# Optimization experiments

Hardware: AMD Instinct MI355X
Metric: run time of the kernel (lower is better)

## Reference

```python
import jax, jax.numpy as jnp
import numpy as np

R = 16
ALPHA = 32
SCALING = ALPHA / R  # 2.0
E = 8
TOP_K = 2


def setup_inputs() -> dict:
    key = jax.random.key(0)
    ks = jax.random.split(key, 5)
    B, S, D = 4, 2048, 4096
    x = jax.random.normal(ks[0], (B, S, D), dtype=jnp.float32)
    base_W = jax.random.normal(ks[1], (D, D), dtype=jnp.float32) * 0.02
    router_W = jax.random.normal(ks[2], (E, D), dtype=jnp.float32) * 0.02
    lora_A = jax.random.normal(ks[3], (E, D, R), dtype=jnp.float32) * 0.02
    lora_B = jax.random.normal(ks[4], (E, R, D), dtype=jnp.float32) * 0.02
    return {"x": x, "base_W": base_W, "router_W": router_W,
            "lora_A": lora_A, "lora_B": lora_B}


def reference(x, base_W, router_W, lora_A, lora_B):
    # base linear: y = x @ W^T  (nn.Linear, bias=False)
    base = jnp.einsum('bsd,od->bso', x, base_W)

    # router logits and top-2 routing (softmax in fp32, as in torch)
    logits = jnp.einsum('bsd,ed->bse', x, router_W)
    probs = jax.nn.softmax(logits.astype(jnp.float32), axis=-1)  # [B,S,E]
    top_vals, top_idx = jax.lax.top_k(probs, TOP_K)               # [B,S,2]
    rw = top_vals / jnp.sum(top_vals, axis=-1, keepdims=True)
    # scatter top-2 weights into dense [B,S,E] combine matrix
    w_dense = jnp.sum(jax.nn.one_hot(top_idx, E, dtype=rw.dtype) * rw[..., None],
                      axis=-2).astype(x.dtype)                    # [B,S,E]

    # expert LoRA: out_n = sum_e w_ne * (x_n @ A_e @ B_e)
    # apply routing weight at rank-r stage (B_e linear => same math),
    # avoiding the [B,S,E,D] intermediate.
    mid = jnp.einsum('bsd,edr->bser', x, lora_A)                  # [B,S,E,r]
    mid = mid * w_dense[..., None]
    inc = jnp.einsum('bser,erd->bsd', mid, lora_B)                # [B,S,D]

    return base + inc * SCALING
```

## Files before the change

kernel.cpp:

```cpp
#include <hip/hip_runtime.h>
#include <math.h>

#define DI __device__ __forceinline__

typedef __attribute__((ext_vector_type(4))) float  f32x4;
typedef __attribute__((ext_vector_type(4))) short  s16x4;
typedef __attribute__((ext_vector_type(8))) short  s16x8;
typedef __attribute__((ext_vector_type(4))) float  ffrag;
typedef s16x8 bfrag;

constexpr int NT = 8192;
constexpr int D  = 4096;
constexpr int NE = 8;
constexpr int KE = 128;
constexpr int KX = D + KE;

DI short f2bf(float f) {
  unsigned u = __builtin_bit_cast(unsigned, f);
  u += 0x7FFFu + ((u >> 16) & 1u);
  return (short)(u >> 16);
}
DI float bf2f(short h) {
  unsigned u = ((unsigned)(unsigned short)h) << 16;
  return __builtin_bit_cast(float, u);
}

#define GLOAD16(gp, lp)                                                        \
  __builtin_amdgcn_global_load_lds(                                            \
      (const __attribute__((address_space(1))) void*)(gp),                     \
      (__attribute__((address_space(3))) void*)(lp), 16, 0, 0)

__global__ void moe_k_detect(const unsigned* __restrict__ x, int* __restrict__ flag) {
  int l = threadIdx.x;
  int cnt = 0;
  for (int i = l; i < 2048; i += 64) {
    unsigned e = (x[i] >> 23) & 0xFFu;
    cnt += (e >= 110u && e <= 140u) ? 1 : 0;
  }
#pragma unroll
  for (int o = 32; o; o >>= 1) cnt += __shfl_xor(cnt, o);
  if (l == 0) flag[0] = (cnt > 1024) ? 0 : 1;
}

__global__ __launch_bounds__(256)
void moe_k_prep(const void* __restrict__ wp, const void* __restrict__ lAp,
                const void* __restrict__ lBp, const int* __restrict__ flag,
                short* __restrict__ Wb, short* __restrict__ Abt) {
  const bool bf = flag[0] != 0;
  int b = blockIdx.x, t = threadIdx.x;
  if (b < 8192) {
    int tid = b * 256 + t;
    int row = tid >> 9;
    int col = (tid & 511) << 3;
    s16x8 o;
    if (!bf) {
      const float* Wf = (const float*)wp;
      f32x4 v0 = *(const f32x4*)&Wf[(size_t)row * 4096 + col];
      f32x4 v1 = *(const f32x4*)&Wf[(size_t)row * 4096 + col + 4];
      o[0] = f2bf(v0[0]); o[1] = f2bf(v0[1]); o[2] = f2bf(v0[2]); o[3] = f2bf(v0[3]);
      o[4] = f2bf(v1[0]); o[5] = f2bf(v1[1]); o[6] = f2bf(v1[2]); o[7] = f2bf(v1[3]);
    } else {
      o = *(const s16x8*)&((const short*)wp)[(size_t)row * 4096 + col];
    }
    *(s16x8*)&Wb[(size_t)row * KX + col] = o;
  } else if (b < 8208) {
    int d = (b - 8192) * 256 + t;
    for (int j0 = 0; j0 < KE; j0 += 8) {
      s16x8 o;
#pragma unroll
      for (int i = 0; i < 8; ++i) {
        float v = bf ? bf2f(((const short*)lBp)[(size_t)(j0 + i) * 4096 + d])
                     : ((const float*)lBp)[(size_t)(j0 + i) * 4096 + d];
        o[i] = f2bf(2.0f * v);
      }
      *(s16x8*)&Wb[(size_t)d * KX + 4096 + j0] = o;
    }
  } else {
    int j = b - 8208;
    int e = j >> 4, r = j & 15;
    for (int d = t; d < 4096; d += 256) {
      size_t src = ((size_t)e * 4096 + d) * 16 + r;
      short v = bf ? ((const short*)lAp)[src] : f2bf(((const float*)lAp)[src]);
      Abt[(size_t)j * 4096 + d] = v;
    }
  }
}

__global__ __launch_bounds__(256)
void moe_k_xrouter(const void* __restrict__ xp, const void* __restrict__ rp,
                   const int* __restrict__ flag, short* __restrict__ Xb,
                   float* __restrict__ wdense) {
  const bool bf = flag[0] != 0;
  int t = threadIdx.x, wv = t >> 6, l = t & 63;
  int n = blockIdx.x * 4 + wv;
  float acc[NE];
#pragma unroll
  for (int e = 0; e < NE; ++e) acc[e] = 0.f;
  const float* xf = (const float*)xp;
  const short* xh = (const short*)xp;
  const float* rf = (const float*)rp;
  const short* rh = (const short*)rp;
  for (int it = 0; it < 16; ++it) {
    int d = it * 256 + l * 4;
    float x0, x1, x2, x3;
    s16x4 xo;
    if (!bf) {
      f32x4 v = *(const f32x4*)&xf[(size_t)n * D + d];
      x0 = v[0]; x1 = v[1]; x2 = v[2]; x3 = v[3];
      xo[0] = f2bf(x0); xo[1] = f2bf(x1); xo[2] = f2bf(x2); xo[3] = f2bf(x3);
    } else {
      xo = *(const s16x4*)&xh[(size_t)n * D + d];
      x0 = bf2f(xo[0]); x1 = bf2f(xo[1]); x2 = bf2f(xo[2]); x3 = bf2f(xo[3]);
    }
    *(s16x4*)&Xb[(size_t)n * KX + d] = xo;
#pragma unroll
    for (int e = 0; e < NE; ++e) {
      if (!bf) {
        f32x4 w = *(const f32x4*)&rf[(size_t)e * D + d];
        acc[e] += x0 * w[0] + x1 * w[1] + x2 * w[2] + x3 * w[3];
      } else {
        s16x4 w = *(const s16x4*)&rh[(size_t)e * D + d];
        acc[e] += x0 * bf2f(w[0]) + x1 * bf2f(w[1]) + x2 * bf2f(w[2]) + x3 * bf2f(w[3]);
      }
    }
  }
#pragma unroll
  for (int e = 0; e < NE; ++e) {
#pragma unroll
    for (int o = 32; o; o >>= 1) acc[e] += __shfl_xor(acc[e], o);
  }
  float m = acc[0];
#pragma unroll
  for (int e = 1; e < NE; ++e) m = fmaxf(m, acc[e]);
  float p[NE];
#pragma unroll
  for (int e = 0; e < NE; ++e) p[e] = __expf(acc[e] - m);
  int i1 = 0; float v1 = p[0];
#pragma unroll
  for (int e = 1; e < NE; ++e) { if (p[e] > v1) { v1 = p[e]; i1 = e; } }
  int i2 = 0; float v2 = -1.f;
#pragma unroll
  for (int e = 0; e < NE; ++e) { if (e != i1 && p[e] > v2) { v2 = p[e]; i2 = e; } }
  float inv = 1.f / (v1 + v2);
  if (l < NE) {
    float w = (l == i1) ? v1 * inv : ((l == i2) ? v2 * inv : 0.f);
    wdense[(size_t)n * NE + l] = w;
  }
}

__global__ __launch_bounds__(256)
void moe_k_mid2(const short* __restrict__ Xb, const short* __restrict__ Abt,
                const float* __restrict__ wdense, short* __restrict__ XbW) {
  __shared__ __align__(16) short LDS[16384];
  const int t = threadIdx.x, l = t & 63, wv = t >> 6;
  const int wr = wv >> 1, wc = wv & 1;
  const int lr = l & 15, kq = l >> 4;
  const int m0 = (blockIdx.x >> 1) * 64;
  const int j0 = (blockIdx.x & 1) * 64;

  ffrag acc[2][2];
#pragma unroll
  for (int i = 0; i < 2; ++i)
#pragma unroll
    for (int j = 0; j < 2; ++j)
#pragma unroll
      for (int q = 0; q < 4; ++q) acc[i][j][q] = 0.f;

  const int srow = t >> 2, sslot = t & 3;
#define MSTAGE(kt_)                                                            \
  do {                                                                         \
    int _k0 = (kt_) * 32, _b = ((kt_) & 3) * 4096;                             \
    GLOAD16(&Xb[(size_t)(m0 + srow) * KX + _k0 + sslot * 8], &LDS[_b + t * 8]);\
    GLOAD16(&Abt[(size_t)(j0 + srow) * 4096 + _k0 + sslot * 8],                \
            &LDS[_b + 2048 + t * 8]);                                          \
  } while (0)

  MSTAGE(0); MSTAGE(1); MSTAGE(2);
  constexpr int NKT = 128;

  for (int kt = 0; kt < NKT; ++kt) {
    if (kt + 2 < NKT)      asm volatile("s_waitcnt vmcnt(4)" ::: "memory");
    else if (kt + 1 < NKT) asm volatile("s_waitcnt vmcnt(2)" ::: "memory");
    else                   asm volatile("s_waitcnt vmcnt(0)" ::: "memory");
    __builtin_amdgcn_s_barrier();
    __builtin_amdgcn_sched_barrier(0);

    const int bufs = (kt & 3) * 4096;
    const short* As = &LDS[bufs + (wr * 32 + lr) * 32 + kq * 8];
    const short* Bs = &LDS[bufs + 2048 + (wc * 32 + lr) * 32 + kq * 8];
    bfrag a0 = *(const bfrag*)&As[0];
    bfrag a1 = *(const bfrag*)&As[512];
    bfrag b0 = *(const bfrag*)&Bs[0];
    bfrag b1 = *(const bfrag*)&Bs[512];
    if (kt + 3 < NKT) MSTAGE(kt + 3);
    asm volatile("" ::: "memory");
    acc[0][0] = __builtin_amdgcn_mfma_f32_16x16x32_bf16(b0, a0, acc[0][0], 0, 0, 0);
    acc[0][1] = __builtin_amdgcn_mfma_f32_16x16x32_bf16(b1, a0, acc[0][1], 0, 0, 0);
    acc[1][0] = __builtin_amdgcn_mfma_f32_16x16x32_bf16(b0, a1, acc[1][0], 0, 0, 0);
    acc[1][1] = __builtin_amdgcn_mfma_f32_16x16x32_bf16(b1, a1, acc[1][1], 0, 0, 0);
  }

#pragma unroll
  for (int m = 0; m < 2; ++m)
#pragma unroll
    for (int n = 0; n < 2; ++n) {
      int gr = m0 + wr * 32 + m * 16 + lr;
      int jb = j0 + wc * 32 + n * 16 + kq * 4;
      int e  = jb >> 4;
      float w = wdense[(size_t)gr * NE + e];
      s16x4 o;
#pragma unroll
      for (int q = 0; q < 4; ++q) o[q] = f2bf(acc[m][n][q] * w);
      *(s16x4*)&XbW[(size_t)gr * KX + 4096 + jb] = o;
    }
#undef MSTAGE
}

__global__ __launch_bounds__(512, 2)
void moe_k_main8(const short* __restrict__ Xb, const short* __restrict__ Wb,
                 const int* __restrict__ flag, void* __restrict__ outp) {
  __shared__ __align__(16) short LDS[65536];
  const int t = threadIdx.x;
  const int l = t & 63;
  const int wv = t >> 6;
  const int wr = wv >> 2;
  const int wc = wv & 3;
  const int lr = l & 15;
  const int kq = l >> 4;

  int wg = blockIdx.x;
  int swz = (wg & 7) * 64 + (wg >> 3);
  const int tm = (swz >> 4) * 256;
  const int tn = (swz & 15) * 256;

  ffrag acc[8][4];
#pragma unroll
  for (int i = 0; i < 8; ++i)
#pragma unroll
    for (int j = 0; j < 4; ++j)
#pragma unroll
      for (int q = 0; q < 4; ++q) acc[i][j][q] = 0.f;

#define STAGE_A(kt_)                                                           \
  do {                                                                         \
    int _k0 = (kt_) * 32, _b = ((kt_) & 3) * 16384;                            \
    _Pragma("unroll")                                                          \
    for (int _i = 0; _i < 2; ++_i) {                                           \
      int _c = _i * 512 + t;                                                   \
      int _r = _c >> 2;                                                        \
      int _kc = (_c & 3) ^ ((_r >> 1) & 3);                                    \
      GLOAD16(&Xb[(size_t)(tm + _r) * KX + _k0 + _kc * 8], &LDS[_b + _c * 8]); \
    }                                                                          \
  } while (0)
#define STAGE_B(kt_)                                                           \
  do {                                                                         \
    int _k0 = (kt_) * 32, _b = ((kt_) & 3) * 16384 + 8192;                     \
    _Pragma("unroll")                                                          \
    for (int _i = 0; _i < 2; ++_i) {                                           \
      int _c = _i * 512 + t;                                                   \
      int _r = _c >> 2;                                                        \
      int _kc = (_c & 3) ^ ((_r >> 1) & 3);                                    \
      GLOAD16(&Wb[(size_t)(tn + _r) * KX + _k0 + _kc * 8], &LDS[_b + _c * 8]); \
    }                                                                          \
  } while (0)

  STAGE_A(0); STAGE_B(0);
  STAGE_A(1); STAGE_B(1);
  STAGE_A(2); STAGE_B(2);

  constexpr int NKT = KX / 32;

  const int kx = kq ^ ((lr >> 1) & 3);
  const int aofs = (wr * 128 + lr) * 32 + kx * 8;
  const int bofs = 8192 + (wc * 64 + lr) * 32 + kx * 8;

#define MFMA_ROW(mi, av)                                                           \
  acc[mi][0] = __builtin_amdgcn_mfma_f32_16x16x32_bf16(b0, av, acc[mi][0], 0, 0, 0); \
  acc[mi][1] = __builtin_amdgcn_mfma_f32_16x16x32_bf16(b1, av, acc[mi][1], 0, 0, 0); \
  acc[mi][2] = __builtin_amdgcn_mfma_f32_16x16x32_bf16(b2, av, acc[mi][2], 0, 0, 0); \
  acc[mi][3] = __builtin_amdgcn_mfma_f32_16x16x32_bf16(b3, av, acc[mi][3], 0, 0, 0);

  for (int kt = 0; kt < NKT; ++kt) {
    if (kt + 2 < NKT)      asm volatile("s_waitcnt vmcnt(8)" ::: "memory");
    else if (kt + 1 < NKT) asm volatile("s_waitcnt vmcnt(4)" ::: "memory");
    else                   asm volatile("s_waitcnt vmcnt(0)" ::: "memory");
    __builtin_amdgcn_s_barrier();
    __builtin_amdgcn_sched_barrier(0);

    const int bufs = (kt & 3) * 16384;
    const short* Ab = &LDS[bufs + aofs];
    const short* Bb = &LDS[bufs + bofs];

    bfrag b0 = *(const bfrag*)&Bb[0];
    bfrag b1 = *(const bfrag*)&Bb[512];
    bfrag b2 = *(const bfrag*)&Bb[1024];
    bfrag b3 = *(const bfrag*)&Bb[1536];
    bfrag a0 = *(const bfrag*)&Ab[0];
    bfrag a1 = *(const bfrag*)&Ab[512];
    bfrag a2 = *(const bfrag*)&Ab[1024];
    bfrag a3 = *(const bfrag*)&Ab[1536];
    if (kt + 3 < NKT) STAGE_A(kt + 3);
    asm volatile("" ::: "memory");
    __builtin_amdgcn_s_barrier();
    __builtin_amdgcn_sched_barrier(0);
    __builtin_amdgcn_s_setprio(1);
    MFMA_ROW(0, a0) MFMA_ROW(1, a1) MFMA_ROW(2, a2) MFMA_ROW(3, a3)
    __builtin_amdgcn_s_setprio(0);

    bfrag a4 = *(const bfrag*)&Ab[2048];
    bfrag a5 = *(const bfrag*)&Ab[2560];
    bfrag a6 = *(const bfrag*)&Ab[3072];
    bfrag a7 = *(const bfrag*)&Ab[3584];
    if (kt + 3 < NKT) STAGE_B(kt + 3);
    asm volatile("" ::: "memory");
    __builtin_amdgcn_s_barrier();
    __builtin_amdgcn_sched_barrier(0);
    __builtin_amdgcn_s_setprio(1);
    MFMA_ROW(4, a4) MFMA_ROW(5, a5) MFMA_ROW(6, a6) MFMA_ROW(7, a7)
    __builtin_amdgcn_s_setprio(0);
  }

  const bool bf = flag[0] != 0;
  float* of = (float*)outp;
  unsigned short* oh = (unsigned short*)outp;
#pragma unroll
  for (int m = 0; m < 8; ++m)
#pragma unroll
    for (int n = 0; n < 4; ++n) {
      int gr = tm + wr * 128 + m * 16 + lr;
      int gc = tn + wc * 64 + n * 16 + kq * 4;
      if (!bf) {
        *(f32x4*)&of[(size_t)gr * D + gc] = acc[m][n];
      } else {
        s16x4 o;
#pragma unroll
        for (int q = 0; q < 4; ++q) o[q] = f2bf(acc[m][n][q]);
        *(s16x4*)&oh[(size_t)gr * D + gc] = o;
      }
    }
#undef STAGE_A
#undef STAGE_B
#undef MFMA_ROW
}

extern "C" void kernel_launch(void* const* d_in, const int* in_sizes, int n_in,
                              void* d_out, int out_size, void* d_ws, size_t ws_size,
                              hipStream_t stream) {
  const void* x  = d_in[0];
  const void* bw = d_in[1];
  const void* rw = d_in[2];
  const void* lA = d_in[3];
  const void* lB = d_in[4];

  char* ws = (char*)d_ws;
  const size_t XB_BYTES  = (size_t)NT * KX * 2;
  const size_t WB_BYTES  = (size_t)D * KX * 2;
  const size_t ABT_BYTES = (size_t)KE * D * 2;
  const size_t WD_BYTES  = (size_t)NT * NE * 4;
  const size_t NEED = 256 + XB_BYTES + WB_BYTES + ABT_BYTES + WD_BYTES;
  if (ws_size < NEED) return;

  int*   flag   = (int*)ws;
  short* Xb     = (short*)(ws + 256);
  short* Wb     = (short*)(ws + 256 + XB_BYTES);
  short* Abt    = (short*)(ws + 256 + XB_BYTES + WB_BYTES);
  float* wdense = (float*)(ws + 256 + XB_BYTES + WB_BYTES + ABT_BYTES);

  hipLaunchKernelGGL(moe_k_detect, dim3(1), dim3(64), 0, stream,
                     (const unsigned*)x, flag);
  hipLaunchKernelGGL(moe_k_prep, dim3(8336), dim3(256), 0, stream,
                     bw, lA, lB, flag, Wb, Abt);
  hipLaunchKernelGGL(moe_k_xrouter, dim3(NT / 4), dim3(256), 0, stream,
                     x, rw, flag, Xb, wdense);
  hipLaunchKernelGGL(moe_k_mid2, dim3(256), dim3(256), 0, stream,
                     Xb, Abt, wdense, Xb);
  hipLaunchKernelGGL(moe_k_main8, dim3(512), dim3(512), 0, stream,
                     Xb, Wb, flag, d_out);
}
```

Measured before the change: 403.7 us.

## Merge prep and router kernels; software-pipeline LDS fragment loads in main GEMM

```diff
diff --git a/kernel.cpp b/kernel.cpp
--- a/kernel.cpp
+++ b/kernel.cpp
@@ -43,9 +43,11 @@
 }
 
 __global__ __launch_bounds__(256)
-void moe_k_prep(const void* __restrict__ wp, const void* __restrict__ lAp,
-                const void* __restrict__ lBp, const int* __restrict__ flag,
-                short* __restrict__ Wb, short* __restrict__ Abt) {
+void moe_k_prep_xr(const void* __restrict__ wp, const void* __restrict__ lAp,
+                   const void* __restrict__ lBp, const void* __restrict__ xp,
+                   const void* __restrict__ rp, const int* __restrict__ flag,
+                   short* __restrict__ Wb, short* __restrict__ Abt,
+                   short* __restrict__ Xb, float* __restrict__ wdense) {
   const bool bf = flag[0] != 0;
   int b = blockIdx.x, t = threadIdx.x;
   if (b < 8192) {
@@ -75,7 +77,7 @@
       }
       *(s16x8*)&Wb[(size_t)d * KX + 4096 + j0] = o;
     }
-  } else {
+  } else if (b < 8336) {
     int j = b - 8208;
     int e = j >> 4, r = j & 15;
     for (int d = t; d < 4096; d += 256) {
@@ -83,68 +85,62 @@
       short v = bf ? ((const short*)lAp)[src] : f2bf(((const float*)lAp)[src]);
       Abt[(size_t)j * 4096 + d] = v;
     }
-  }
-}
-
-__global__ __launch_bounds__(256)
-void moe_k_xrouter(const void* __restrict__ xp, const void* __restrict__ rp,
-                   const int* __restrict__ flag, short* __restrict__ Xb,
-                   float* __restrict__ wdense) {
-  const bool bf = flag[0] != 0;
-  int t = threadIdx.x, wv = t >> 6, l = t & 63;
-  int n = blockIdx.x * 4 + wv;
-  float acc[NE];
-#pragma unroll
-  for (int e = 0; e < NE; ++e) acc[e] = 0.f;
-  const float* xf = (const float*)xp;
-  const short* xh = (const short*)xp;
-  const float* rf = (const float*)rp;
-  const short* rh = (const short*)rp;
-  for (int it = 0; it < 16; ++it) {
-    int d = it * 256 + l * 4;
-    float x0, x1, x2, x3;
-    s16x4 xo;
-    if (!bf) {
-      f32x4 v = *(const f32x4*)&xf[(size_t)n * D + d];
-      x0 = v[0]; x1 = v[1]; x2 = v[2]; x3 = v[3];
-      xo[0] = f2bf(x0); xo[1] = f2bf(x1); xo[2] = f2bf(x2); xo[3] = f2bf(x3);
-    } else {
-      xo = *(const s16x4*)&xh[(size_t)n * D + d];
-      x0 = bf2f(xo[0]); x1 = bf2f(xo[1]); x2 = bf2f(xo[2]); x3 = bf2f(xo[3]);
-    }
-    *(s16x4*)&Xb[(size_t)n * KX + d] = xo;
+  } else {
+    int wv = t >> 6, l = t & 63;
+    int n = (b - 8336) * 4 + wv;
+    float acc[NE];
+#pragma unroll
+    for (int e = 0; e < NE; ++e) acc[e] = 0.f;
+    const float* xf = (const float*)xp;
+    const short* xh = (const short*)xp;
+    const float* rf = (const float*)rp;
+    const short* rh = (const short*)rp;
+    for (int it = 0; it < 16; ++it) {
+      int d = it * 256 + l * 4;
+      float x0, x1, x2, x3;
+      s16x4 xo;
+      if (!bf) {
+        f32x4 v = *(const f32x4*)&xf[(size_t)n * D + d];
+        x0 = v[0]; x1 = v[1]; x2 = v[2]; x3 = v[3];
+        xo[0] = f2bf(x0); xo[1] = f2bf(x1); xo[2] = f2bf(x2); xo[3] = f2bf(x3);
+      } else {
+        xo = *(const s16x4*)&xh[(size_t)n * D + d];
+        x0 = bf2f(xo[0]); x1 = bf2f(xo[1]); x2 = bf2f(xo[2]); x3 = bf2f(xo[3]);
+      }
+      *(s16x4*)&Xb[(size_t)n * KX + d] = xo;
+#pragma unroll
+      for (int e = 0; e < NE; ++e) {
+        if (!bf) {
+          f32x4 w = *(const f32x4*)&rf[(size_t)e * D + d];
+          acc[e] += x0 * w[0] + x1 * w[1] + x2 * w[2] + x3 * w[3];
+        } else {
+          s16x4 w = *(const s16x4*)&rh[(size_t)e * D + d];
+          acc[e] += x0 * bf2f(w[0]) + x1 * bf2f(w[1]) + x2 * bf2f(w[2]) + x3 * bf2f(w[3]);
+        }
+      }
+    }
 #pragma unroll
     for (int e = 0; e < NE; ++e) {
-      if (!bf) {
-        f32x4 w = *(const f32x4*)&rf[(size_t)e * D + d];
-        acc[e] += x0 * w[0] + x1 * w[1] + x2 * w[2] + x3 * w[3];
-      } else {
-        s16x4 w = *(const s16x4*)&rh[(size_t)e * D + d];
-        acc[e] += x0 * bf2f(w[0]) + x1 * bf2f(w[1]) + x2 * bf2f(w[2]) + x3 * bf2f(w[3]);
-      }
-    }
-  }
-#pragma unroll
-  for (int e = 0; e < NE; ++e) {
-#pragma unroll
-    for (int o = 32; o; o >>= 1) acc[e] += __shfl_xor(acc[e], o);
-  }
-  float m = acc[0];
-#pragma unroll
-  for (int e = 1; e < NE; ++e) m = fmaxf(m, acc[e]);
-  float p[NE];
-#pragma unroll
-  for (int e = 0; e < NE; ++e) p[e] = __expf(acc[e] - m);
-  int i1 = 0; float v1 = p[0];
-#pragma unroll
-  for (int e = 1; e < NE; ++e) { if (p[e] > v1) { v1 = p[e]; i1 = e; } }
-  int i2 = 0; float v2 = -1.f;
-#pragma unroll
-  for (int e = 0; e < NE; ++e) { if (e != i1 && p[e] > v2) { v2 = p[e]; i2 = e; } }
-  float inv = 1.f / (v1 + v2);
-  if (l < NE) {
-    float w = (l == i1) ? v1 * inv : ((l == i2) ? v2 * inv : 0.f);
-    wdense[(size_t)n * NE + l] = w;
+#pragma unroll
+      for (int o = 32; o; o >>= 1) acc[e] += __shfl_xor(acc[e], o);
+    }
+    float m = acc[0];
+#pragma unroll
+    for (int e = 1; e < NE; ++e) m = fmaxf(m, acc[e]);
+    float p[NE];
+#pragma unroll
+    for (int e = 0; e < NE; ++e) p[e] = __expf(acc[e] - m);
+    int i1 = 0; float v1 = p[0];
+#pragma unroll
+    for (int e = 1; e < NE; ++e) { if (p[e] > v1) { v1 = p[e]; i1 = e; } }
+    int i2 = 0; float v2 = -1.f;
+#pragma unroll
+    for (int e = 0; e < NE; ++e) { if (e != i1 && p[e] > v2) { v2 = p[e]; i2 = e; } }
+    float inv = 1.f / (v1 + v2);
+    if (l < NE) {
+      float w = (l == i1) ? v1 * inv : ((l == i2) ? v2 * inv : 0.f);
+      wdense[(size_t)n * NE + l] = w;
+    }
   }
 }
 
@@ -274,50 +270,67 @@
   const int aofs = (wr * 128 + lr) * 32 + kx * 8;
   const int bofs = 8192 + (wc * 64 + lr) * 32 + kx * 8;
 
-#define MFMA_ROW(mi, av)                                                           \
-  acc[mi][0] = __builtin_amdgcn_mfma_f32_16x16x32_bf16(b0, av, acc[mi][0], 0, 0, 0); \
-  acc[mi][1] = __builtin_amdgcn_mfma_f32_16x16x32_bf16(b1, av, acc[mi][1], 0, 0, 0); \
-  acc[mi][2] = __builtin_amdgcn_mfma_f32_16x16x32_bf16(b2, av, acc[mi][2], 0, 0, 0); \
-  acc[mi][3] = __builtin_amdgcn_mfma_f32_16x16x32_bf16(b3, av, acc[mi][3], 0, 0, 0);
-
-  for (int kt = 0; kt < NKT; ++kt) {
-    if (kt + 2 < NKT)      asm volatile("s_waitcnt vmcnt(8)" ::: "memory");
-    else if (kt + 1 < NKT) asm volatile("s_waitcnt vmcnt(4)" ::: "memory");
-    else                   asm volatile("s_waitcnt vmcnt(0)" ::: "memory");
-    __builtin_amdgcn_s_barrier();
-    __builtin_amdgcn_sched_barrier(0);
-
-    const int bufs = (kt & 3) * 16384;
-    const short* Ab = &LDS[bufs + aofs];
-    const short* Bb = &LDS[bufs + bofs];
-
-    bfrag b0 = *(const bfrag*)&Bb[0];
-    bfrag b1 = *(const bfrag*)&Bb[512];
-    bfrag b2 = *(const bfrag*)&Bb[1024];
-    bfrag b3 = *(const bfrag*)&Bb[1536];
-    bfrag a0 = *(const bfrag*)&Ab[0];
-    bfrag a1 = *(const bfrag*)&Ab[512];
-    bfrag a2 = *(const bfrag*)&Ab[1024];
-    bfrag a3 = *(const bfrag*)&Ab[1536];
-    if (kt + 3 < NKT) STAGE_A(kt + 3);
-    asm volatile("" ::: "memory");
-    __builtin_amdgcn_s_barrier();
-    __builtin_amdgcn_sched_barrier(0);
-    __builtin_amdgcn_s_setprio(1);
-    MFMA_ROW(0, a0) MFMA_ROW(1, a1) MFMA_ROW(2, a2) MFMA_ROW(3, a3)
-    __builtin_amdgcn_s_setprio(0);
-
-    bfrag a4 = *(const bfrag*)&Ab[2048];
-    bfrag a5 = *(const bfrag*)&Ab[2560];
-    bfrag a6 = *(const bfrag*)&Ab[3072];
-    bfrag a7 = *(const bfrag*)&Ab[3584];
-    if (kt + 3 < NKT) STAGE_B(kt + 3);
-    asm volatile("" ::: "memory");
-    __builtin_amdgcn_s_barrier();
-    __builtin_amdgcn_sched_barrier(0);
-    __builtin_amdgcn_s_setprio(1);
-    MFMA_ROW(4, a4) MFMA_ROW(5, a5) MFMA_ROW(6, a6) MFMA_ROW(7, a7)
-    __builtin_amdgcn_s_setprio(0);
+  bfrag bA[4], aA[8], bB[4], aB[8];
+
+  asm volatile("s_waitcnt vmcnt(4)" ::: "memory");
+  __builtin_amdgcn_s_barrier();
+  asm volatile("" ::: "memory");
+  {
+    const short* Ab0 = &LDS[aofs];
+    const short* Bb0 = &LDS[bofs];
+#pragma unroll
+    for (int i = 0; i < 4; ++i) bA[i] = *(const bfrag*)&Bb0[i * 512];
+#pragma unroll
+    for (int i = 0; i < 4; ++i) aA[i] = *(const bfrag*)&Ab0[i * 512];
+  }
+
+#define TILE_BODY(kt_, CURB, CURA, NXTB, NXTA, LAST)                           \
+  {                                                                            \
+    const int _slc = ((kt_) & 3) * 16384;                                      \
+    const short* _AbC = &LDS[_slc + aofs];                                     \
+    _Pragma("unroll")                                                          \
+    for (int _i = 0; _i < 4; ++_i)                                             \
+      CURA[4 + _i] = *(const bfrag*)&_AbC[2048 + _i * 512];                    \
+    if ((kt_) + 3 < NKT) STAGE_A((kt_) + 3);                                   \
+    __builtin_amdgcn_sched_barrier(0);                                         \
+    __builtin_amdgcn_s_setprio(1);                                             \
+    _Pragma("unroll")                                                          \
+    for (int _m = 0; _m < 4; ++_m)                                             \
+      _Pragma("unroll")                                                        \
+      for (int _n = 0; _n < 4; ++_n)                                           \
+        acc[_m][_n] = __builtin_amdgcn_mfma_f32_16x16x32_bf16(                 \
+            CURB[_n], CURA[_m], acc[_m][_n], 0, 0, 0);                         \
+    __builtin_amdgcn_s_setprio(0);                                             \
+    if (!(LAST)) {                                                             \
+      const int _sln = (((kt_) + 1) & 3) * 16384;                              \
+      const short* _AbN = &LDS[_sln + aofs];                                   \
+      const short* _BbN = &LDS[_sln + bofs];                                   \
+      _Pragma("unroll")                                                        \
+      for (int _i = 0; _i < 4; ++_i) NXTB[_i] = *(const bfrag*)&_BbN[_i * 512];\
+      _Pragma("unroll")                                                        \
+      for (int _i = 0; _i < 4; ++_i) NXTA[_i] = *(const bfrag*)&_AbN[_i * 512];\
+    }                                                                          \
+    if ((kt_) + 3 < NKT) STAGE_B((kt_) + 3);                                   \
+    __builtin_amdgcn_sched_barrier(0);                                         \
+    __builtin_amdgcn_s_setprio(1);                                             \
+    _Pragma("unroll")                                                          \
+    for (int _m = 4; _m < 8; ++_m)                                             \
+      _Pragma("unroll")                                                        \
+      for (int _n = 0; _n < 4; ++_n)                                           \
+        acc[_m][_n] = __builtin_amdgcn_mfma_f32_16x16x32_bf16(                 \
+            CURB[_n], CURA[_m], acc[_m][_n], 0, 0, 0);                         \
+    __builtin_amdgcn_s_setprio(0);                                             \
+    if (!(LAST)) {                                                             \
+      if ((kt_) + 4 < NKT) { asm volatile("s_waitcnt vmcnt(4)" ::: "memory"); }\
+      else                 { asm volatile("s_waitcnt vmcnt(0)" ::: "memory"); }\
+      __builtin_amdgcn_s_barrier();                                            \
+      asm volatile("" ::: "memory");                                          \
+    }                                                                          \
+  }
+
+  for (int kt = 0; kt < NKT; kt += 2) {
+    TILE_BODY(kt,     bA, aA, bB, aB, false);
+    TILE_BODY(kt + 1, bB, aB, bA, aA, (kt + 2 >= NKT));
   }
 
   const bool bf = flag[0] != 0;
@@ -340,7 +353,7 @@
     }
 #undef STAGE_A
 #undef STAGE_B
-#undef MFMA_ROW
+#undef TILE_BODY
 }
 
 extern "C" void kernel_launch(void* const* d_in, const int* in_sizes, int n_in,
@@ -368,10 +381,8 @@
 
   hipLaunchKernelGGL(moe_k_detect, dim3(1), dim3(64), 0, stream,
                      (const unsigned*)x, flag);
-  hipLaunchKernelGGL(moe_k_prep, dim3(8336), dim3(256), 0, stream,
-                     bw, lA, lB, flag, Wb, Abt);
-  hipLaunchKernelGGL(moe_k_xrouter, dim3(NT / 4), dim3(256), 0, stream,
-                     x, rw, flag, Xb, wdense);
+  hipLaunchKernelGGL(moe_k_prep_xr, dim3(10384), dim3(256), 0, stream,
+                     bw, lA, lB, x, rw, flag, Wb, Abt, Xb, wdense);
   hipLaunchKernelGGL(moe_k_mid2, dim3(256), dim3(256), 0, stream,
                      Xb, Abt, wdense, Xb);
   hipLaunchKernelGGL(moe_k_main8, dim3(512), dim3(512), 0, stream,
```

After: 385.0 us. -4.6%, faster.

## Merge prep and router kernels; split main GEMM loop into four interleaved phases

Applied to the files above, without the earlier changes.

```diff
diff --git a/kernel.cpp b/kernel.cpp
--- a/kernel.cpp
+++ b/kernel.cpp
@@ -43,9 +43,11 @@
 }
 
 __global__ __launch_bounds__(256)
-void moe_k_prep(const void* __restrict__ wp, const void* __restrict__ lAp,
-                const void* __restrict__ lBp, const int* __restrict__ flag,
-                short* __restrict__ Wb, short* __restrict__ Abt) {
+void moe_k_prep_xr(const void* __restrict__ wp, const void* __restrict__ lAp,
+                   const void* __restrict__ lBp, const void* __restrict__ xp,
+                   const void* __restrict__ rp, const int* __restrict__ flag,
+                   short* __restrict__ Wb, short* __restrict__ Abt,
+                   short* __restrict__ Xb, float* __restrict__ wdense) {
   const bool bf = flag[0] != 0;
   int b = blockIdx.x, t = threadIdx.x;
   if (b < 8192) {
@@ -75,7 +77,7 @@
       }
       *(s16x8*)&Wb[(size_t)d * KX + 4096 + j0] = o;
     }
-  } else {
+  } else if (b < 8336) {
     int j = b - 8208;
     int e = j >> 4, r = j & 15;
     for (int d = t; d < 4096; d += 256) {
@@ -83,68 +85,62 @@
       short v = bf ? ((const short*)lAp)[src] : f2bf(((const float*)lAp)[src]);
       Abt[(size_t)j * 4096 + d] = v;
     }
-  }
-}
-
-__global__ __launch_bounds__(256)
-void moe_k_xrouter(const void* __restrict__ xp, const void* __restrict__ rp,
-                   const int* __restrict__ flag, short* __restrict__ Xb,
-                   float* __restrict__ wdense) {
-  const bool bf = flag[0] != 0;
-  int t = threadIdx.x, wv = t >> 6, l = t & 63;
-  int n = blockIdx.x * 4 + wv;
-  float acc[NE];
-#pragma unroll
-  for (int e = 0; e < NE; ++e) acc[e] = 0.f;
-  const float* xf = (const float*)xp;
-  const short* xh = (const short*)xp;
-  const float* rf = (const float*)rp;
-  const short* rh = (const short*)rp;
-  for (int it = 0; it < 16; ++it) {
-    int d = it * 256 + l * 4;
-    float x0, x1, x2, x3;
-    s16x4 xo;
-    if (!bf) {
-      f32x4 v = *(const f32x4*)&xf[(size_t)n * D + d];
-      x0 = v[0]; x1 = v[1]; x2 = v[2]; x3 = v[3];
-      xo[0] = f2bf(x0); xo[1] = f2bf(x1); xo[2] = f2bf(x2); xo[3] = f2bf(x3);
-    } else {
-      xo = *(const s16x4*)&xh[(size_t)n * D + d];
-      x0 = bf2f(xo[0]); x1 = bf2f(xo[1]); x2 = bf2f(xo[2]); x3 = bf2f(xo[3]);
-    }
-    *(s16x4*)&Xb[(size_t)n * KX + d] = xo;
+  } else {
+    int wv = t >> 6, l = t & 63;
+    int n = (b - 8336) * 4 + wv;
+    float acc[NE];
+#pragma unroll
+    for (int e = 0; e < NE; ++e) acc[e] = 0.f;
+    const float* xf = (const float*)xp;
+    const short* xh = (const short*)xp;
+    const float* rf = (const float*)rp;
+    const short* rh = (const short*)rp;
+    for (int it = 0; it < 16; ++it) {
+      int d = it * 256 + l * 4;
+      float x0, x1, x2, x3;
+      s16x4 xo;
+      if (!bf) {
+        f32x4 v = *(const f32x4*)&xf[(size_t)n * D + d];
+        x0 = v[0]; x1 = v[1]; x2 = v[2]; x3 = v[3];
+        xo[0] = f2bf(x0); xo[1] = f2bf(x1); xo[2] = f2bf(x2); xo[3] = f2bf(x3);
+      } else {
+        xo = *(const s16x4*)&xh[(size_t)n * D + d];
+        x0 = bf2f(xo[0]); x1 = bf2f(xo[1]); x2 = bf2f(xo[2]); x3 = bf2f(xo[3]);
+      }
+      *(s16x4*)&Xb[(size_t)n * KX + d] = xo;
+#pragma unroll
+      for (int e = 0; e < NE; ++e) {
+        if (!bf) {
+          f32x4 w = *(const f32x4*)&rf[(size_t)e * D + d];
+          acc[e] += x0 * w[0] + x1 * w[1] + x2 * w[2] + x3 * w[3];
+        } else {
+          s16x4 w = *(const s16x4*)&rh[(size_t)e * D + d];
+          acc[e] += x0 * bf2f(w[0]) + x1 * bf2f(w[1]) + x2 * bf2f(w[2]) + x3 * bf2f(w[3]);
+        }
+      }
+    }
 #pragma unroll
     for (int e = 0; e < NE; ++e) {
-      if (!bf) {
-        f32x4 w = *(const f32x4*)&rf[(size_t)e * D + d];
-        acc[e] += x0 * w[0] + x1 * w[1] + x2 * w[2] + x3 * w[3];
-      } else {
-        s16x4 w = *(const s16x4*)&rh[(size_t)e * D + d];
-        acc[e] += x0 * bf2f(w[0]) + x1 * bf2f(w[1]) + x2 * bf2f(w[2]) + x3 * bf2f(w[3]);
-      }
-    }
-  }
-#pragma unroll
-  for (int e = 0; e < NE; ++e) {
-#pragma unroll
-    for (int o = 32; o; o >>= 1) acc[e] += __shfl_xor(acc[e], o);
-  }
-  float m = acc[0];
-#pragma unroll
-  for (int e = 1; e < NE; ++e) m = fmaxf(m, acc[e]);
-  float p[NE];
-#pragma unroll
-  for (int e = 0; e < NE; ++e) p[e] = __expf(acc[e] - m);
-  int i1 = 0; float v1 = p[0];
-#pragma unroll
-  for (int e = 1; e < NE; ++e) { if (p[e] > v1) { v1 = p[e]; i1 = e; } }
-  int i2 = 0; float v2 = -1.f;
-#pragma unroll
-  for (int e = 0; e < NE; ++e) { if (e != i1 && p[e] > v2) { v2 = p[e]; i2 = e; } }
-  float inv = 1.f / (v1 + v2);
-  if (l < NE) {
-    float w = (l == i1) ? v1 * inv : ((l == i2) ? v2 * inv : 0.f);
-    wdense[(size_t)n * NE + l] = w;
+#pragma unroll
+      for (int o = 32; o; o >>= 1) acc[e] += __shfl_xor(acc[e], o);
+    }
+    float m = acc[0];
+#pragma unroll
+    for (int e = 1; e < NE; ++e) m = fmaxf(m, acc[e]);
+    float p[NE];
+#pragma unroll
+    for (int e = 0; e < NE; ++e) p[e] = __expf(acc[e] - m);
+    int i1 = 0; float v1 = p[0];
+#pragma unroll
+    for (int e = 1; e < NE; ++e) { if (p[e] > v1) { v1 = p[e]; i1 = e; } }
+    int i2 = 0; float v2 = -1.f;
+#pragma unroll
+    for (int e = 0; e < NE; ++e) { if (e != i1 && p[e] > v2) { v2 = p[e]; i2 = e; } }
+    float inv = 1.f / (v1 + v2);
+    if (l < NE) {
+      float w = (l == i1) ? v1 * inv : ((l == i2) ? v2 * inv : 0.f);
+      wdense[(size_t)n * NE + l] = w;
+    }
   }
 }
 
@@ -241,32 +237,23 @@
 #pragma unroll
       for (int q = 0; q < 4; ++q) acc[i][j][q] = 0.f;
 
-#define STAGE_A(kt_)                                                           \
+#define STAGE_ONE(kt_, base_, src_, half_)                                     \
   do {                                                                         \
-    int _k0 = (kt_) * 32, _b = ((kt_) & 3) * 16384;                            \
-    _Pragma("unroll")                                                          \
-    for (int _i = 0; _i < 2; ++_i) {                                           \
-      int _c = _i * 512 + t;                                                   \
-      int _r = _c >> 2;                                                        \
-      int _kc = (_c & 3) ^ ((_r >> 1) & 3);                                    \
-      GLOAD16(&Xb[(size_t)(tm + _r) * KX + _k0 + _kc * 8], &LDS[_b + _c * 8]); \
-    }                                                                          \
+    int _k0 = (kt_) * 32, _b = ((kt_) & 3) * 16384 + (base_);                  \
+    int _c = (half_) * 512 + t;                                                \
+    int _r = _c >> 2;                                                          \
+    int _kc = (_c & 3) ^ ((_r >> 1) & 3);                                      \
+    GLOAD16(&src_[(size_t)((base_ ? tn : tm) + _r) * KX + _k0 + _kc * 8],      \
+            &LDS[_b + _c * 8]);                                                \
   } while (0)
-#define STAGE_B(kt_)                                                           \
-  do {                                                                         \
-    int _k0 = (kt_) * 32, _b = ((kt_) & 3) * 16384 + 8192;                     \
-    _Pragma("unroll")                                                          \
-    for (int _i = 0; _i < 2; ++_i) {                                           \
-      int _c = _i * 512 + t;                                                   \
-      int _r = _c >> 2;                                                        \
-      int _kc = (_c & 3) ^ ((_r >> 1) & 3);                                    \
-      GLOAD16(&Wb[(size_t)(tn + _r) * KX + _k0 + _kc * 8], &LDS[_b + _c * 8]); \
-    }                                                                          \
-  } while (0)
-
-  STAGE_A(0); STAGE_B(0);
-  STAGE_A(1); STAGE_B(1);
-  STAGE_A(2); STAGE_B(2);
+#define STAGE_A1(kt_) STAGE_ONE(kt_, 0,    Xb, 0)
+#define STAGE_A2(kt_) STAGE_ONE(kt_, 0,    Xb, 1)
+#define STAGE_B1(kt_) STAGE_ONE(kt_, 8192, Wb, 0)
+#define STAGE_B2(kt_) STAGE_ONE(kt_, 8192, Wb, 1)
+
+  STAGE_A1(0); STAGE_A2(0); STAGE_B1(0); STAGE_B2(0);
+  STAGE_A1(1); STAGE_A2(1); STAGE_B1(1); STAGE_B2(1);
+  STAGE_A1(2); STAGE_A2(2); STAGE_B1(2); STAGE_B2(2);
 
   constexpr int NKT = KX / 32;
 
@@ -274,11 +261,8 @@
   const int aofs = (wr * 128 + lr) * 32 + kx * 8;
   const int bofs = 8192 + (wc * 64 + lr) * 32 + kx * 8;
 
-#define MFMA_ROW(mi, av)                                                           \
-  acc[mi][0] = __builtin_amdgcn_mfma_f32_16x16x32_bf16(b0, av, acc[mi][0], 0, 0, 0); \
-  acc[mi][1] = __builtin_amdgcn_mfma_f32_16x16x32_bf16(b1, av, acc[mi][1], 0, 0, 0); \
-  acc[mi][2] = __builtin_amdgcn_mfma_f32_16x16x32_bf16(b2, av, acc[mi][2], 0, 0, 0); \
-  acc[mi][3] = __builtin_amdgcn_mfma_f32_16x16x32_bf16(b3, av, acc[mi][3], 0, 0, 0);
+#define MFMA1(m_, n_, av_, bv_)                                                \
+  acc[m_][n_] = __builtin_amdgcn_mfma_f32_16x16x32_bf16(bv_, av_, acc[m_][n_], 0, 0, 0);
 
   for (int kt = 0; kt < NKT; ++kt) {
     if (kt + 2 < NKT)      asm volatile("s_waitcnt vmcnt(8)" ::: "memory");
@@ -293,31 +277,60 @@
 
     bfrag b0 = *(const bfrag*)&Bb[0];
     bfrag b1 = *(const bfrag*)&Bb[512];
-    bfrag b2 = *(const bfrag*)&Bb[1024];
-    bfrag b3 = *(const bfrag*)&Bb[1536];
     bfrag a0 = *(const bfrag*)&Ab[0];
     bfrag a1 = *(const bfrag*)&Ab[512];
     bfrag a2 = *(const bfrag*)&Ab[1024];
     bfrag a3 = *(const bfrag*)&Ab[1536];
-    if (kt + 3 < NKT) STAGE_A(kt + 3);
-    asm volatile("" ::: "memory");
-    __builtin_amdgcn_s_barrier();
+    if (kt + 3 < NKT) STAGE_A1(kt + 3);
+    __builtin_amdgcn_s_barrier();
+    asm volatile("s_waitcnt lgkmcnt(0)" ::: "memory");
     __builtin_amdgcn_sched_barrier(0);
     __builtin_amdgcn_s_setprio(1);
-    MFMA_ROW(0, a0) MFMA_ROW(1, a1) MFMA_ROW(2, a2) MFMA_ROW(3, a3)
+    MFMA1(0, 0, a0, b0) MFMA1(0, 1, a0, b1)
+    MFMA1(1, 0, a1, b0) MFMA1(1, 1, a1, b1)
+    MFMA1(2, 0, a2, b0) MFMA1(2, 1, a2, b1)
+    MFMA1(3, 0, a3, b0) MFMA1(3, 1, a3, b1)
     __builtin_amdgcn_s_setprio(0);
+    __builtin_amdgcn_sched_barrier(0);
 
     bfrag a4 = *(const bfrag*)&Ab[2048];
     bfrag a5 = *(const bfrag*)&Ab[2560];
     bfrag a6 = *(const bfrag*)&Ab[3072];
     bfrag a7 = *(const bfrag*)&Ab[3584];
-    if (kt + 3 < NKT) STAGE_B(kt + 3);
-    asm volatile("" ::: "memory");
-    __builtin_amdgcn_s_barrier();
+    if (kt + 3 < NKT) STAGE_A2(kt + 3);
+    __builtin_amdgcn_s_barrier();
+    asm volatile("s_waitcnt lgkmcnt(0)" ::: "memory");
     __builtin_amdgcn_sched_barrier(0);
     __builtin_amdgcn_s_setprio(1);
-    MFMA_ROW(4, a4) MFMA_ROW(5, a5) MFMA_ROW(6, a6) MFMA_ROW(7, a7)
+    MFMA1(4, 0, a4, b0) MFMA1(4, 1, a4, b1)
+    MFMA1(5, 0, a5, b0) MFMA1(5, 1, a5, b1)
+    MFMA1(6, 0, a6, b0) MFMA1(6, 1, a6, b1)
+    MFMA1(7, 0, a7, b0) MFMA1(7, 1, a7, b1)
     __builtin_amdgcn_s_setprio(0);
+    __builtin_amdgcn_sched_barrier(0);
+
+    bfrag b2 = *(const bfrag*)&Bb[1024];
+    bfrag b3 = *(const bfrag*)&Bb[1536];
+    if (kt + 3 < NKT) STAGE_B1(kt + 3);
+    __builtin_amdgcn_s_barrier();
+    asm volatile("s_waitcnt lgkmcnt(0)" ::: "memory");
+    __builtin_amdgcn_sched_barrier(0);
+    __builtin_amdgcn_s_setprio(1);
+    MFMA1(4, 2, a4, b2) MFMA1(4, 3, a4, b3)
+    MFMA1(5, 2, a5, b2) MFMA1(5, 3, a5, b3)
+    MFMA1(6, 2, a6, b2) MFMA1(6, 3, a6, b3)
+    MFMA1(7, 2, a7, b2) MFMA1(7, 3, a7, b3)
+    __builtin_amdgcn_s_setprio(0);
+    __builtin_amdgcn_sched_barrier(0);
+
+    if (kt + 3 < NKT) STAGE_B2(kt + 3);
+    __builtin_amdgcn_s_setprio(1);
+    MFMA1(0, 2, a0, b2) MFMA1(0, 3, a0, b3)
+    MFMA1(1, 2, a1, b2) MFMA1(1, 3, a1, b3)
+    MFMA1(2, 2, a2, b2) MFMA1(2, 3, a2, b3)
+    MFMA1(3, 2, a3, b2) MFMA1(3, 3, a3, b3)
+    __builtin_amdgcn_s_setprio(0);
+    __builtin_amdgcn_sched_barrier(0);
   }
 
   const bool bf = flag[0] != 0;
@@ -338,9 +351,12 @@
         *(s16x4*)&oh[(size_t)gr * D + gc] = o;
       }
     }
-#undef STAGE_A
-#undef STAGE_B
-#undef MFMA_ROW
+#undef STAGE_ONE
+#undef STAGE_A1
+#undef STAGE_A2
+#undef STAGE_B1
+#undef STAGE_B2
+#undef MFMA1
 }
 
 extern "C" void kernel_launch(void* const* d_in, const int* in_sizes, int n_in,
@@ -368,10 +384,8 @@
 
   hipLaunchKernelGGL(moe_k_detect, dim3(1), dim3(64), 0, stream,
                      (const unsigned*)x, flag);
-  hipLaunchKernelGGL(moe_k_prep, dim3(8336), dim3(256), 0, stream,
-                     bw, lA, lB, flag, Wb, Abt);
-  hipLaunchKernelGGL(moe_k_xrouter, dim3(NT / 4), dim3(256), 0, stream,
-                     x, rw, flag, Xb, wdense);
+  hipLaunchKernelGGL(moe_k_prep_xr, dim3(10384), dim3(256), 0, stream,
+                     bw, lA, lB, x, rw, flag, Wb, Abt, Xb, wdense);
   hipLaunchKernelGGL(moe_k_mid2, dim3(256), dim3(256), 0, stream,
                      Xb, Abt, wdense, Xb);
   hipLaunchKernelGGL(moe_k_main8, dim3(512), dim3(512), 0, stream,
```

New measurement: 394.1 us. 1.02x faster.

## Switch main GEMM to 32x32x16 MFMA, drop inner barriers, fuse router prep

Applied to the files above, without the earlier changes.

```diff
diff --git a/kernel.cpp b/kernel.cpp
--- a/kernel.cpp
+++ b/kernel.cpp
@@ -3,10 +3,11 @@
 
 #define DI __device__ __forceinline__
 
-typedef __attribute__((ext_vector_type(4))) float  f32x4;
-typedef __attribute__((ext_vector_type(4))) short  s16x4;
-typedef __attribute__((ext_vector_type(8))) short  s16x8;
-typedef __attribute__((ext_vector_type(4))) float  ffrag;
+typedef __attribute__((ext_vector_type(4)))  float f32x4;
+typedef __attribute__((ext_vector_type(4)))  short s16x4;
+typedef __attribute__((ext_vector_type(8)))  short s16x8;
+typedef __attribute__((ext_vector_type(4)))  float ffrag;
+typedef __attribute__((ext_vector_type(16))) float ffrag16;
 typedef s16x8 bfrag;
 
 constexpr int NT = 8192;
@@ -43,9 +44,11 @@
 }
 
 __global__ __launch_bounds__(256)
-void moe_k_prep(const void* __restrict__ wp, const void* __restrict__ lAp,
-                const void* __restrict__ lBp, const int* __restrict__ flag,
-                short* __restrict__ Wb, short* __restrict__ Abt) {
+void moe_k_prep_xr(const void* __restrict__ wp, const void* __restrict__ lAp,
+                   const void* __restrict__ lBp, const void* __restrict__ xp,
+                   const void* __restrict__ rp, const int* __restrict__ flag,
+                   short* __restrict__ Wb, short* __restrict__ Abt,
+                   short* __restrict__ Xb, float* __restrict__ wdense) {
   const bool bf = flag[0] != 0;
   int b = blockIdx.x, t = threadIdx.x;
   if (b < 8192) {
@@ -75,7 +78,7 @@
       }
       *(s16x8*)&Wb[(size_t)d * KX + 4096 + j0] = o;
     }
-  } else {
+  } else if (b < 8336) {
     int j = b - 8208;
     int e = j >> 4, r = j & 15;
     for (int d = t; d < 4096; d += 256) {
@@ -83,68 +86,62 @@
       short v = bf ? ((const short*)lAp)[src] : f2bf(((const float*)lAp)[src]);
       Abt[(size_t)j * 4096 + d] = v;
     }
-  }
-}
-
-__global__ __launch_bounds__(256)
-void moe_k_xrouter(const void* __restrict__ xp, const void* __restrict__ rp,
-                   const int* __restrict__ flag, short* __restrict__ Xb,
-                   float* __restrict__ wdense) {
-  const bool bf = flag[0] != 0;
-  int t = threadIdx.x, wv = t >> 6, l = t & 63;
-  int n = blockIdx.x * 4 + wv;
-  float acc[NE];
-#pragma unroll
-  for (int e = 0; e < NE; ++e) acc[e] = 0.f;
-  const float* xf = (const float*)xp;
-  const short* xh = (const short*)xp;
-  const float* rf = (const float*)rp;
-  const short* rh = (const short*)rp;
-  for (int it = 0; it < 16; ++it) {
-    int d = it * 256 + l * 4;
-    float x0, x1, x2, x3;
-    s16x4 xo;
-    if (!bf) {
-      f32x4 v = *(const f32x4*)&xf[(size_t)n * D + d];
-      x0 = v[0]; x1 = v[1]; x2 = v[2]; x3 = v[3];
-      xo[0] = f2bf(x0); xo[1] = f2bf(x1); xo[2] = f2bf(x2); xo[3] = f2bf(x3);
-    } else {
-      xo = *(const s16x4*)&xh[(size_t)n * D + d];
-      x0 = bf2f(xo[0]); x1 = bf2f(xo[1]); x2 = bf2f(xo[2]); x3 = bf2f(xo[3]);
-    }
-    *(s16x4*)&Xb[(size_t)n * KX + d] = xo;
+  } else {
+    int wv = t >> 6, l = t & 63;
+    int n = (b - 8336) * 4 + wv;
+    float acc[NE];
+#pragma unroll
+    for (int e = 0; e < NE; ++e) acc[e] = 0.f;
+    const float* xf = (const float*)xp;
+    const short* xh = (const short*)xp;
+    const float* rf = (const float*)rp;
+    const short* rh = (const short*)rp;
+    for (int it = 0; it < 16; ++it) {
+      int d = it * 256 + l * 4;
+      float x0, x1, x2, x3;
+      s16x4 xo;
+      if (!bf) {
+        f32x4 v = *(const f32x4*)&xf[(size_t)n * D + d];
+        x0 = v[0]; x1 = v[1]; x2 = v[2]; x3 = v[3];
+        xo[0] = f2bf(x0); xo[1] = f2bf(x1); xo[2] = f2bf(x2); xo[3] = f2bf(x3);
+      } else {
+        xo = *(const s16x4*)&xh[(size_t)n * D + d];
+        x0 = bf2f(xo[0]); x1 = bf2f(xo[1]); x2 = bf2f(xo[2]); x3 = bf2f(xo[3]);
+      }
+      *(s16x4*)&Xb[(size_t)n * KX + d] = xo;
+#pragma unroll
+      for (int e = 0; e < NE; ++e) {
+        if (!bf) {
+          f32x4 w = *(const f32x4*)&rf[(size_t)e * D + d];
+          acc[e] += x0 * w[0] + x1 * w[1] + x2 * w[2] + x3 * w[3];
+        } else {
+          s16x4 w = *(const s16x4*)&rh[(size_t)e * D + d];
+          acc[e] += x0 * bf2f(w[0]) + x1 * bf2f(w[1]) + x2 * bf2f(w[2]) + x3 * bf2f(w[3]);
+        }
+      }
+    }
 #pragma unroll
     for (int e = 0; e < NE; ++e) {
-      if (!bf) {
-        f32x4 w = *(const f32x4*)&rf[(size_t)e * D + d];
-        acc[e] += x0 * w[0] + x1 * w[1] + x2 * w[2] + x3 * w[3];
-      } else {
-        s16x4 w = *(const s16x4*)&rh[(size_t)e * D + d];
-        acc[e] += x0 * bf2f(w[0]) + x1 * bf2f(w[1]) + x2 * bf2f(w[2]) + x3 * bf2f(w[3]);
-      }
-    }
-  }
-#pragma unroll
-  for (int e = 0; e < NE; ++e) {
-#pragma unroll
-    for (int o = 32; o; o >>= 1) acc[e] += __shfl_xor(acc[e], o);
-  }
-  float m = acc[0];
-#pragma unroll
-  for (int e = 1; e < NE; ++e) m = fmaxf(m, acc[e]);
-  float p[NE];
-#pragma unroll
-  for (int e = 0; e < NE; ++e) p[e] = __expf(acc[e] - m);
-  int i1 = 0; float v1 = p[0];
-#pragma unroll
-  for (int e = 1; e < NE; ++e) { if (p[e] > v1) { v1 = p[e]; i1 = e; } }
-  int i2 = 0; float v2 = -1.f;
-#pragma unroll
-  for (int e = 0; e < NE; ++e) { if (e != i1 && p[e] > v2) { v2 = p[e]; i2 = e; } }
-  float inv = 1.f / (v1 + v2);
-  if (l < NE) {
-    float w = (l == i1) ? v1 * inv : ((l == i2) ? v2 * inv : 0.f);
-    wdense[(size_t)n * NE + l] = w;
+#pragma unroll
+      for (int o = 32; o; o >>= 1) acc[e] += __shfl_xor(acc[e], o);
+    }
+    float m = acc[0];
+#pragma unroll
+    for (int e = 1; e < NE; ++e) m = fmaxf(m, acc[e]);
+    float p[NE];
+#pragma unroll
+    for (int e = 0; e < NE; ++e) p[e] = __expf(acc[e] - m);
+    int i1 = 0; float v1 = p[0];
+#pragma unroll
+    for (int e = 1; e < NE; ++e) { if (p[e] > v1) { v1 = p[e]; i1 = e; } }
+    int i2 = 0; float v2 = -1.f;
+#pragma unroll
+    for (int e = 0; e < NE; ++e) { if (e != i1 && p[e] > v2) { v2 = p[e]; i2 = e; } }
+    float inv = 1.f / (v1 + v2);
+    if (l < NE) {
+      float w = (l == i1) ? v1 * inv : ((l == i2) ? v2 * inv : 0.f);
+      wdense[(size_t)n * NE + l] = w;
+    }
   }
 }
 
@@ -225,21 +222,21 @@
   const int wv = t >> 6;
   const int wr = wv >> 2;
   const int wc = wv & 3;
-  const int lr = l & 15;
-  const int kq = l >> 4;
+  const int la = l & 31;
+  const int hi = l >> 5;
 
   int wg = blockIdx.x;
   int swz = (wg & 7) * 64 + (wg >> 3);
   const int tm = (swz >> 4) * 256;
   const int tn = (swz & 15) * 256;
 
-  ffrag acc[8][4];
-#pragma unroll
-  for (int i = 0; i < 8; ++i)
-#pragma unroll
-    for (int j = 0; j < 4; ++j)
-#pragma unroll
-      for (int q = 0; q < 4; ++q) acc[i][j][q] = 0.f;
+  ffrag16 acc[4][2];
+#pragma unroll
+  for (int i = 0; i < 4; ++i)
+#pragma unroll
+    for (int j = 0; j < 2; ++j)
+#pragma unroll
+      for (int q = 0; q < 16; ++q) acc[i][j][q] = 0.f;
 
 #define STAGE_A(kt_)                                                           \
   do {                                                                         \
@@ -270,15 +267,12 @@
 
   constexpr int NKT = KX / 32;
 
-  const int kx = kq ^ ((lr >> 1) & 3);
-  const int aofs = (wr * 128 + lr) * 32 + kx * 8;
-  const int bofs = 8192 + (wc * 64 + lr) * 32 + kx * 8;
-
-#define MFMA_ROW(mi, av)                                                           \
-  acc[mi][0] = __builtin_amdgcn_mfma_f32_16x16x32_bf16(b0, av, acc[mi][0], 0, 0, 0); \
-  acc[mi][1] = __builtin_amdgcn_mfma_f32_16x16x32_bf16(b1, av, acc[mi][1], 0, 0, 0); \
-  acc[mi][2] = __builtin_amdgcn_mfma_f32_16x16x32_bf16(b2, av, acc[mi][2], 0, 0, 0); \
-  acc[mi][3] = __builtin_amdgcn_mfma_f32_16x16x32_bf16(b3, av, acc[mi][3], 0, 0, 0);
+  const int s0 = hi ^ ((la >> 1) & 3);
+  const int aoff = (wr * 128 + la) * 32 + s0 * 8;
+  const int boff = 8192 + (wc * 64 + la) * 32 + s0 * 8;
+
+#define MM(m_, n_, bv_, av_)                                                   \
+  acc[m_][n_] = __builtin_amdgcn_mfma_f32_32x32x16_bf16(bv_, av_, acc[m_][n_], 0, 0, 0);
 
   for (int kt = 0; kt < NKT; ++kt) {
     if (kt + 2 < NKT)      asm volatile("s_waitcnt vmcnt(8)" ::: "memory");
@@ -288,35 +282,37 @@
     __builtin_amdgcn_sched_barrier(0);
 
     const int bufs = (kt & 3) * 16384;
-    const short* Ab = &LDS[bufs + aofs];
-    const short* Bb = &LDS[bufs + bofs];
-
-    bfrag b0 = *(const bfrag*)&Bb[0];
-    bfrag b1 = *(const bfrag*)&Bb[512];
-    bfrag b2 = *(const bfrag*)&Bb[1024];
-    bfrag b3 = *(const bfrag*)&Bb[1536];
-    bfrag a0 = *(const bfrag*)&Ab[0];
-    bfrag a1 = *(const bfrag*)&Ab[512];
-    bfrag a2 = *(const bfrag*)&Ab[1024];
-    bfrag a3 = *(const bfrag*)&Ab[1536];
+    const int aP = bufs + aoff;
+    const int bP = bufs + boff;
+
+    bfrag b0 = *(const bfrag*)&LDS[bP];
+    bfrag b1 = *(const bfrag*)&LDS[bP + 1024];
+    bfrag a0 = *(const bfrag*)&LDS[aP];
+    bfrag a1 = *(const bfrag*)&LDS[aP + 1024];
+    bfrag a2 = *(const bfrag*)&LDS[aP + 2048];
+    bfrag a3 = *(const bfrag*)&LDS[aP + 3072];
     if (kt + 3 < NKT) STAGE_A(kt + 3);
-    asm volatile("" ::: "memory");
-    __builtin_amdgcn_s_barrier();
     __builtin_amdgcn_sched_barrier(0);
     __builtin_amdgcn_s_setprio(1);
-    MFMA_ROW(0, a0) MFMA_ROW(1, a1) MFMA_ROW(2, a2) MFMA_ROW(3, a3)
+    MM(0, 0, b0, a0) MM(0, 1, b1, a0)
+    MM(1, 0, b0, a1) MM(1, 1, b1, a1)
+    MM(2, 0, b0, a2) MM(2, 1, b1, a2)
+    MM(3, 0, b0, a3) MM(3, 1, b1, a3)
     __builtin_amdgcn_s_setprio(0);
 
-    bfrag a4 = *(const bfrag*)&Ab[2048];
-    bfrag a5 = *(const bfrag*)&Ab[2560];
-    bfrag a6 = *(const bfrag*)&Ab[3072];
-    bfrag a7 = *(const bfrag*)&Ab[3584];
+    bfrag c0 = *(const bfrag*)&LDS[bP ^ 16];
+    bfrag c1 = *(const bfrag*)&LDS[(bP + 1024) ^ 16];
+    bfrag e0 = *(const bfrag*)&LDS[aP ^ 16];
+    bfrag e1 = *(const bfrag*)&LDS[(aP + 1024) ^ 16];
+    bfrag e2 = *(const bfrag*)&LDS[(aP + 2048) ^ 16];
+    bfrag e3 = *(const bfrag*)&LDS[(aP + 3072) ^ 16];
     if (kt + 3 < NKT) STAGE_B(kt + 3);
-    asm volatile("" ::: "memory");
-    __builtin_amdgcn_s_barrier();
     __builtin_amdgcn_sched_barrier(0);
     __builtin_amdgcn_s_setprio(1);
-    MFMA_ROW(4, a4) MFMA_ROW(5, a5) MFMA_ROW(6, a6) MFMA_ROW(7, a7)
+    MM(0, 0, c0, e0) MM(0, 1, c1, e0)
+    MM(1, 0, c0, e1) MM(1, 1, c1, e1)
+    MM(2, 0, c0, e2) MM(2, 1, c1, e2)
+    MM(3, 0, c0, e3) MM(3, 1, c1, e3)
     __builtin_amdgcn_s_setprio(0);
   }
 
@@ -324,23 +320,30 @@
   float* of = (float*)outp;
   unsigned short* oh = (unsigned short*)outp;
 #pragma unroll
-  for (int m = 0; m < 8; ++m)
-#pragma unroll
-    for (int n = 0; n < 4; ++n) {
-      int gr = tm + wr * 128 + m * 16 + lr;
-      int gc = tn + wc * 64 + n * 16 + kq * 4;
-      if (!bf) {
-        *(f32x4*)&of[(size_t)gr * D + gc] = acc[m][n];
-      } else {
-        s16x4 o;
-#pragma unroll
-        for (int q = 0; q < 4; ++q) o[q] = f2bf(acc[m][n][q]);
-        *(s16x4*)&oh[(size_t)gr * D + gc] = o;
+  for (int m = 0; m < 4; ++m)
+#pragma unroll
+    for (int n = 0; n < 2; ++n) {
+      int gr = tm + wr * 128 + m * 32 + la;
+      int cb = tn + wc * 64 + n * 32 + hi * 4;
+#pragma unroll
+      for (int g = 0; g < 4; ++g) {
+        int gc = cb + g * 8;
+        if (!bf) {
+          f32x4 v;
+#pragma unroll
+          for (int q = 0; q < 4; ++q) v[q] = acc[m][n][g * 4 + q];
+          *(f32x4*)&of[(size_t)gr * D + gc] = v;
+        } else {
+          s16x4 o;
+#pragma unroll
+          for (int q = 0; q < 4; ++q) o[q] = f2bf(acc[m][n][g * 4 + q]);
+          *(s16x4*)&oh[(size_t)gr * D + gc] = o;
+        }
       }
     }
 #undef STAGE_A
 #undef STAGE_B
-#undef MFMA_ROW
+#undef MM
 }
 
 extern "C" void kernel_launch(void* const* d_in, const int* in_sizes, int n_in,
@@ -368,10 +371,8 @@
 
   hipLaunchKernelGGL(moe_k_detect, dim3(1), dim3(64), 0, stream,
                      (const unsigned*)x, flag);
-  hipLaunchKernelGGL(moe_k_prep, dim3(8336), dim3(256), 0, stream,
-                     bw, lA, lB, flag, Wb, Abt);
-  hipLaunchKernelGGL(moe_k_xrouter, dim3(NT / 4), dim3(256), 0, stream,
-                     x, rw, flag, Xb, wdense);
+  hipLaunchKernelGGL(moe_k_prep_xr, dim3(10384), dim3(256), 0, stream,
+                     bw, lA, lB, x, rw, flag, Wb, Abt, Xb, wdense);
   hipLaunchKernelGGL(moe_k_mid2, dim3(256), dim3(256), 0, stream,
                      Xb, Abt, wdense, Xb);
   hipLaunchKernelGGL(moe_k_main8, dim3(512), dim3(512), 0, stream,
```

Result: slower. 420.9 us (+4.3%).
